# Kernel tuning notes

Measured on AMD Instinct MI355X. Metric: run time of the kernel, lower is better.

The kernel has to match this reference:

```python
import jax, jax.numpy as jnp
import numpy as np

EMBED = 1024
HEADS = 16
HEAD_DIM = EMBED // HEADS


def setup_inputs() -> dict:
    key = jax.random.key(0)
    k_x, k_q, k_k, k_v, k_o, k_b = jax.random.split(key, 6)
    s = 1.0 / np.sqrt(EMBED)
    return {
        "x": jax.random.normal(k_x, (4, 2048, EMBED), dtype=jnp.float32),
        "Wq": jax.random.uniform(k_q, (EMBED, EMBED), jnp.float32, -s, s),
        "Wk": jax.random.uniform(k_k, (EMBED, EMBED), jnp.float32, -s, s),
        "Wv": jax.random.uniform(k_v, (EMBED, EMBED), jnp.float32, -s, s),
        "Wo": jax.random.uniform(k_o, (EMBED, EMBED), jnp.float32, -s, s),
        "bo": jax.random.uniform(k_b, (EMBED,), jnp.float32, -s, s),
    }


def reference(x, Wq, Wk, Wv, Wo, bo):
    B, S, E = x.shape
    H, D = HEADS, HEAD_DIM
    # torch nn.Linear: y = x @ W.T
    q = (x @ Wq.T).reshape(B, S, H, D).transpose(0, 2, 1, 3)  # [B,H,S,D]
    k = (x @ Wk.T).reshape(B, S, H, D).transpose(0, 2, 1, 3)
    v = (x @ Wv.T).reshape(B, S, H, D).transpose(0, 2, 1, 3)
    # NOTE: module scales by sqrt(embed_size), not sqrt(head_dim)
    scores = jnp.einsum("bhqd,bhkd->bhqk", q, k) / jnp.sqrt(jnp.float32(E))
    causal = jnp.triu(jnp.ones((S, S), dtype=bool), k=1)
    scores = jnp.where(causal, -jnp.inf, scores)
    attn = jax.nn.softmax(scores, axis=-1)
    out = jnp.einsum("bhqk,bhkd->bhqd", attn, v)  # [B,H,S,D]
    out = out.transpose(0, 2, 1, 3).reshape(B, S, E)
    return out @ Wo.T + bo
```

## Files before the change

### kernel.cpp

```cpp
#include <hip/hip_runtime.h>


#define E_DIM 1024
#define S_LEN 2048
#define BATCH 4
#define NHEAD 16
#define HDIM  64

using short8 = __attribute__((ext_vector_type(8))) short;
using f32x4  = __attribute__((ext_vector_type(4))) float;

#define GLD16(gp, lp) __builtin_amdgcn_global_load_lds( \
    (const __attribute__((address_space(1))) void*)(gp), \
    (__attribute__((address_space(3))) void*)(lp), 16, 0, 0)

__device__ inline unsigned short f2bf(float f) {
    unsigned int u = __builtin_bit_cast(unsigned int, f);
    u += 0x7FFFu + ((u >> 16) & 1u);
    return (unsigned short)(u >> 16);
}

__global__ __launch_bounds__(256) void cvt_all(
        const float* __restrict__ x,  const float* __restrict__ wq,
        const float* __restrict__ wk, const float* __restrict__ wv,
        const float* __restrict__ wo,
        unsigned short* __restrict__ xb, unsigned short* __restrict__ wb) {
    const int bid = blockIdx.x;
    const float* src;
    unsigned short* dst;
    int blk;
    if (bid < 8192) { src = x; dst = xb; blk = bid; }
    else {
        const int wsel = (bid - 8192) >> 10;
        blk = (bid - 8192) & 1023;
        src = (wsel == 0) ? wq : (wsel == 1) ? wk : (wsel == 2) ? wv : wo;
        dst = wb + (size_t)wsel * 1048576;
    }
    const int i = (blk * 256 + threadIdx.x) * 4;
    float4 v = *reinterpret_cast<const float4*>(src + i);
    ushort4 o;
    o.x = f2bf(v.x); o.y = f2bf(v.y); o.z = f2bf(v.z); o.w = f2bf(v.w);
    *reinterpret_cast<ushort4*>(dst + i) = o;
}

__global__ __launch_bounds__(256) void gemm_qkv(
        const unsigned short* __restrict__ xb,
        const unsigned short* __restrict__ wb,
        unsigned short* __restrict__ qkv) {
    const int z = blockIdx.z;
    const unsigned short* Bw = wb + (size_t)z * (E_DIM * E_DIM);
    unsigned short* Out = qkv + (size_t)z * ((size_t)BATCH * NHEAD * S_LEN * HDIM);
    const int m0 = blockIdx.x * 128, n0 = blockIdx.y * 128;
    const int tid = threadIdx.x;
    const int lane = tid & 63, w = tid >> 6;
    const int wm = w >> 1, wn = w & 1;
    const int col = lane & 15, hi = lane >> 4;

    __shared__ __align__(16) unsigned short Alds[128 * 32];
    __shared__ __align__(16) unsigned short Blds[128 * 32];

    const int srow = tid >> 2;
    const int sc8  = (tid & 3) * 8;
    const int wofs = w * 512;

    f32x4 acc[4][4] = {};

    for (int kt = 0; kt < E_DIM / 32; ++kt) {
        const int k0 = kt * 32;
        GLD16(xb + (size_t)(m0 + srow) * E_DIM + k0 + sc8,       &Alds[wofs]);
        GLD16(xb + (size_t)(m0 + 64 + srow) * E_DIM + k0 + sc8,  &Alds[2048 + wofs]);
        GLD16(Bw + (size_t)(n0 + srow) * E_DIM + k0 + sc8,       &Blds[wofs]);
        GLD16(Bw + (size_t)(n0 + 64 + srow) * E_DIM + k0 + sc8,  &Blds[2048 + wofs]);
        __syncthreads();
        short8 af[4], bf[4];
#pragma unroll
        for (int mt = 0; mt < 4; ++mt)
            af[mt] = *reinterpret_cast<const short8*>(&Alds[(wm * 64 + mt * 16 + col) * 32 + hi * 8]);
#pragma unroll
        for (int nt = 0; nt < 4; ++nt)
            bf[nt] = *reinterpret_cast<const short8*>(&Blds[(wn * 64 + nt * 16 + col) * 32 + hi * 8]);
#pragma unroll
        for (int mt = 0; mt < 4; ++mt)
#pragma unroll
            for (int nt = 0; nt < 4; ++nt)
                acc[mt][nt] = __builtin_amdgcn_mfma_f32_16x16x32_bf16(af[mt], bf[nt], acc[mt][nt], 0, 0, 0);
        __syncthreads();
    }

    const float scale = (z == 0) ? (0.03125f * 1.44269504f) : 1.0f;
#pragma unroll
    for (int mt = 0; mt < 4; ++mt) {
#pragma unroll
        for (int nt = 0; nt < 4; ++nt) {
#pragma unroll
            for (int b = 0; b < 4; ++b) {
                int m = m0 + wm * 64 + mt * 16 + hi * 4 + b;
                int n = n0 + wn * 64 + nt * 16 + col;
                int bidx = m >> 11, s = m & 2047;
                int h = n >> 6, d = n & 63;
                size_t off = (((size_t)(bidx * NHEAD + h)) * S_LEN + s) * HDIM + d;
                Out[off] = f2bf(acc[mt][nt][b] * scale);
            }
        }
    }
}

__global__ __launch_bounds__(512, 4) void attn_fwd(
        const unsigned short* __restrict__ Q,
        const unsigned short* __restrict__ K,
        const unsigned short* __restrict__ V,
        unsigned short* __restrict__ Out) {
    const int g = blockIdx.x;
    const int p = g >> 6;
    const int bh = (g & 7) + ((g >> 3) & 7) * 8;
    const int b_idx = bh >> 4, h = bh & 15;
    const int tid = threadIdx.x, lane = tid & 63, w = tid >> 6;
    const int col = lane & 15, hi = lane >> 4;

    const unsigned short* Qb = Q + (size_t)bh * (S_LEN * HDIM);
    const unsigned short* Kb = K + (size_t)bh * (S_LEN * HDIM);
    const unsigned short* Vb = V + (size_t)bh * (S_LEN * HDIM);

    __shared__ __align__(16) unsigned short Klds[64 * 64];
    __shared__ __align__(16) unsigned short Vt[64 * 64];
    __shared__ __align__(16) unsigned short Plds[8][16 * 64];
    unsigned short* Pl = &Plds[w][0];

    const int kr = tid >> 3, kc8 = (tid & 7) * 8;
    const int ksw = kc8 ^ ((kr & 7) << 3);
    const int vr = tid & 63, vc8 = (tid >> 6) * 8;

#pragma unroll
    for (int pass = 0; pass < 2; ++pass) {
        const int qt = pass ? (15 - p) : p;
        const int nt = 2 * qt + 2;
        const int q0 = qt * 128 + w * 16;

        short8 qf0, qf1;
        {
            const unsigned short* qrow = Qb + (size_t)(q0 + col) * HDIM;
            qf0 = *reinterpret_cast<const short8*>(qrow + hi * 8);
            qf1 = *reinterpret_cast<const short8*>(qrow + 32 + hi * 8);
        }

        f32x4 acc[4] = {};
        float mrun[4], lrun[4];
#pragma unroll
        for (int b = 0; b < 4; ++b) { mrun[b] = -INFINITY; lrun[b] = 0.f; }

        short8 pk = *reinterpret_cast<const short8*>(Kb + (size_t)kr * HDIM + kc8);
        short8 pv = *reinterpret_cast<const short8*>(Vb + (size_t)vr * HDIM + vc8);

        for (int t = 0; t < nt; ++t) {
            const int kv0 = t * 64;
            __syncthreads();
            *reinterpret_cast<short8*>(&Klds[kr * 64 + ksw]) = pk;
#pragma unroll
            for (int j = 0; j < 8; ++j) {
                const int d0 = vc8 + j;
                Vt[d0 * 64 + (vr ^ ((d0 & 7) << 3))] = (unsigned short)pv[j];
            }
            if (t < nt - 1) {
                const int kn = kv0 + 64;
                pk = *reinterpret_cast<const short8*>(Kb + (size_t)(kn + kr) * HDIM + kc8);
                pv = *reinterpret_cast<const short8*>(Vb + (size_t)(kn + vr) * HDIM + vc8);
            }
            __syncthreads();

            if (kv0 <= q0 + 15) {
                f32x4 s[4];
                __builtin_amdgcn_s_setprio(1);
#pragma unroll
                for (int kc = 0; kc < 4; ++kc) {
                    const int row = kc * 16 + col;
                    const int sw = (row & 7) << 3;
                    const unsigned short* kb = Klds + row * 64;
                    short8 kf0 = *reinterpret_cast<const short8*>(kb + ((hi * 8) ^ sw));
                    short8 kf1 = *reinterpret_cast<const short8*>(kb + ((32 + hi * 8) ^ sw));
                    f32x4 z4 = {0.f, 0.f, 0.f, 0.f};
                    z4 = __builtin_amdgcn_mfma_f32_16x16x32_bf16(qf0, kf0, z4, 0, 0, 0);
                    s[kc] = __builtin_amdgcn_mfma_f32_16x16x32_bf16(qf1, kf1, z4, 0, 0, 0);
                }
                __builtin_amdgcn_s_setprio(0);

                if (kv0 + 63 > q0) {
#pragma unroll
                    for (int kc = 0; kc < 4; ++kc) {
                        int kg = kv0 + kc * 16 + col;
#pragma unroll
                        for (int b = 0; b < 4; ++b) {
                            int qg = q0 + hi * 4 + b;
                            if (kg > qg) s[kc][b] = -INFINITY;
                        }
                    }
                }

                float vb[4];
#pragma unroll
                for (int b = 0; b < 4; ++b) {
                    float v = fmaxf(fmaxf(s[0][b], s[1][b]), fmaxf(s[2][b], s[3][b]));
                    v = fmaxf(v, __shfl_xor(v, 1));
                    v = fmaxf(v, __shfl_xor(v, 2));
                    v = fmaxf(v, __shfl_xor(v, 4));
                    v = fmaxf(v, __shfl_xor(v, 8));
                    vb[b] = v;
                }
                bool grow = (vb[0] > mrun[0] + 11.5f) || (vb[1] > mrun[1] + 11.5f) ||
                            (vb[2] > mrun[2] + 11.5f) || (vb[3] > mrun[3] + 11.5f);
                if (__any(grow)) {
#pragma unroll
                    for (int b = 0; b < 4; ++b) {
                        float mnew = fmaxf(mrun[b], vb[b]);
                        float fac = exp2f(mrun[b] - mnew);
                        mrun[b] = mnew;
                        lrun[b] *= fac;
#pragma unroll
                        for (int dt = 0; dt < 4; ++dt) acc[dt][b] *= fac;
                    }
                }
#pragma unroll
                for (int kc = 0; kc < 4; ++kc) {
                    const int c = kc * 16 + col;
#pragma unroll
                    for (int b = 0; b < 4; ++b) {
                        float pp = exp2f(s[kc][b] - mrun[b]);
                        lrun[b] += pp;
                        const int r = hi * 4 + b;
                        Pl[r * 64 + (c ^ ((r & 7) << 3))] = f2bf(pp);
                    }
                }
                const int psw = (col & 7) << 3;
                short8 pf0 = *reinterpret_cast<const short8*>(Pl + col * 64 + ((hi * 8) ^ psw));
                short8 pf1 = *reinterpret_cast<const short8*>(Pl + col * 64 + ((32 + hi * 8) ^ psw));

                __builtin_amdgcn_s_setprio(1);
#pragma unroll
                for (int dt = 0; dt < 4; ++dt) {
                    const int row = dt * 16 + col;
                    const int sw = (row & 7) << 3;
                    const unsigned short* vbp = Vt + row * 64;
                    short8 vf0 = *reinterpret_cast<const short8*>(vbp + ((hi * 8) ^ sw));
                    short8 vf1 = *reinterpret_cast<const short8*>(vbp + ((32 + hi * 8) ^ sw));
                    acc[dt] = __builtin_amdgcn_mfma_f32_16x16x32_bf16(pf0, vf0, acc[dt], 0, 0, 0);
                    acc[dt] = __builtin_amdgcn_mfma_f32_16x16x32_bf16(pf1, vf1, acc[dt], 0, 0, 0);
                }
                __builtin_amdgcn_s_setprio(0);
            }
        }

#pragma unroll
        for (int b = 0; b < 4; ++b) {
            float l = lrun[b];
            l += __shfl_xor(l, 1);
            l += __shfl_xor(l, 2);
            l += __shfl_xor(l, 4);
            l += __shfl_xor(l, 8);
            float inv = 1.0f / l;
            int qg = q0 + hi * 4 + b;
#pragma unroll
            for (int dt = 0; dt < 4; ++dt) {
                size_t off = ((size_t)(b_idx * S_LEN + qg)) * E_DIM + h * HDIM + dt * 16 + col;
                Out[off] = f2bf(acc[dt][b] * inv);
            }
        }
    }
}

__global__ __launch_bounds__(256) void gemm_out(
        const unsigned short* __restrict__ Ab,
        const unsigned short* __restrict__ Bw,
        const float* __restrict__ bias,
        float* __restrict__ Out) {
    const int m0 = blockIdx.x * 128, n0 = blockIdx.y * 128;
    const int tid = threadIdx.x;
    const int lane = tid & 63, w = tid >> 6;
    const int wm = w >> 1, wn = w & 1;
    const int col = lane & 15, hi = lane >> 4;

    __shared__ __align__(16) unsigned short Alds[128 * 32];
    __shared__ __align__(16) unsigned short Blds[128 * 32];

    const int srow = tid >> 2;
    const int sc8  = (tid & 3) * 8;
    const int wofs = w * 512;

    f32x4 acc[4][4] = {};

    for (int kt = 0; kt < E_DIM / 32; ++kt) {
        const int k0 = kt * 32;
        GLD16(Ab + (size_t)(m0 + srow) * E_DIM + k0 + sc8,       &Alds[wofs]);
        GLD16(Ab + (size_t)(m0 + 64 + srow) * E_DIM + k0 + sc8,  &Alds[2048 + wofs]);
        GLD16(Bw + (size_t)(n0 + srow) * E_DIM + k0 + sc8,       &Blds[wofs]);
        GLD16(Bw + (size_t)(n0 + 64 + srow) * E_DIM + k0 + sc8,  &Blds[2048 + wofs]);
        __syncthreads();
        short8 af[4], bf[4];
#pragma unroll
        for (int mt = 0; mt < 4; ++mt)
            af[mt] = *reinterpret_cast<const short8*>(&Alds[(wm * 64 + mt * 16 + col) * 32 + hi * 8]);
#pragma unroll
        for (int nt = 0; nt < 4; ++nt)
            bf[nt] = *reinterpret_cast<const short8*>(&Blds[(wn * 64 + nt * 16 + col) * 32 + hi * 8]);
#pragma unroll
        for (int mt = 0; mt < 4; ++mt)
#pragma unroll
            for (int nt = 0; nt < 4; ++nt)
                acc[mt][nt] = __builtin_amdgcn_mfma_f32_16x16x32_bf16(af[mt], bf[nt], acc[mt][nt], 0, 0, 0);
        __syncthreads();
    }

#pragma unroll
    for (int mt = 0; mt < 4; ++mt) {
#pragma unroll
        for (int nt = 0; nt < 4; ++nt) {
#pragma unroll
            for (int b = 0; b < 4; ++b) {
                int m = m0 + wm * 64 + mt * 16 + hi * 4 + b;
                int n = n0 + wn * 64 + nt * 16 + col;
                Out[(size_t)m * E_DIM + n] = acc[mt][nt][b] + bias[n];
            }
        }
    }
}

extern "C" void kernel_launch(void* const* d_in, const int* in_sizes, int n_in,
                              void* d_out, int out_size, void* d_ws, size_t ws_size,
                              hipStream_t stream) {
    const float* x  = (const float*)d_in[0];
    const float* Wq = (const float*)d_in[1];
    const float* Wk = (const float*)d_in[2];
    const float* Wv = (const float*)d_in[3];
    const float* Wo = (const float*)d_in[4];
    const float* bo = (const float*)d_in[5];
    float* out = (float*)d_out;

    unsigned short* ws   = (unsigned short*)d_ws;
    unsigned short* xb   = ws;
    unsigned short* wb   = xb + (size_t)8192 * 1024;
    unsigned short* qkv  = wb + (size_t)4 * 1024 * 1024;
    unsigned short* attn = qkv + (size_t)3 * 8192 * 1024;

    cvt_all<<<12288, 256, 0, stream>>>(x, Wq, Wk, Wv, Wo, xb, wb);
    gemm_qkv<<<dim3(64, 8, 3), 256, 0, stream>>>(xb, wb, qkv);
    attn_fwd<<<512, 512, 0, stream>>>(qkv, qkv + 8388608, qkv + 2 * 8388608, attn);
    gemm_out<<<dim3(64, 8), 256, 0, stream>>>(attn, wb + 3 * 1048576, bo, out);
}
```

Before: 196.5 us.

## Switch attention to 32x32x16 MFMA with transposed S and register P

Rewrites the attention kernel to compute S^T and O^T with 32x32x16 bf16 MFMAs, so each of 4 waves owns 32 query rows in a 256-thread block. The softmax row statistics become per-lane values, which removes most cross-lane shuffle reductions. P is repacked into MFMA operands through lane-xor-32 shuffles and packed bf16 conversion instead of a round trip through LDS. The P LDS buffer is dropped and the output uses packed 32-bit stores. In exchange, registers per thread go up and there are fewer threads per block to load K and V tiles.

New measurement: 196.9 us. Within noise of the previous version (+0.2%).

```diff
diff --git a/kernel.cpp b/kernel.cpp
--- a/kernel.cpp
+++ b/kernel.cpp
@@ -9,6 +9,8 @@
 
 using short8 = __attribute__((ext_vector_type(8))) short;
 using f32x4  = __attribute__((ext_vector_type(4))) float;
+using f32x16 = __attribute__((ext_vector_type(16))) float;
+using i32x4  = __attribute__((ext_vector_type(4))) int;
 
 #define GLD16(gp, lp) __builtin_amdgcn_global_load_lds( \
     (const __attribute__((address_space(1))) void*)(gp), \
@@ -18,6 +20,12 @@
     unsigned int u = __builtin_bit_cast(unsigned int, f);
     u += 0x7FFFu + ((u >> 16) & 1u);
     return (unsigned short)(u >> 16);
+}
+
+__device__ inline unsigned int cvt_pk_bf16(float a, float b) {
+    unsigned int r;
+    asm("v_cvt_pk_bf16_f32 %0, %1, %2" : "=v"(r) : "v"(a), "v"(b));
+    return r;
 }
 
 __global__ __launch_bounds__(256) void cvt_all(
@@ -105,7 +113,7 @@
     }
 }
 
-__global__ __launch_bounds__(512, 4) void attn_fwd(
+__global__ __launch_bounds__(256, 4) void attn_fwd(
         const unsigned short* __restrict__ Q,
         const unsigned short* __restrict__ K,
         const unsigned short* __restrict__ V,
@@ -115,7 +123,9 @@
     const int bh = (g & 7) + ((g >> 3) & 7) * 8;
     const int b_idx = bh >> 4, h = bh & 15;
     const int tid = threadIdx.x, lane = tid & 63, w = tid >> 6;
-    const int col = lane & 15, hi = lane >> 4;
+    const int l31 = lane & 31, b5 = lane >> 5;
+    const bool lo32 = (b5 == 0);
+    const int rsw = (l31 & 7) << 3;
 
     const unsigned short* Qb = Q + (size_t)bh * (S_LEN * HDIM);
     const unsigned short* Kb = K + (size_t)bh * (S_LEN * HDIM);
@@ -123,8 +133,6 @@
 
     __shared__ __align__(16) unsigned short Klds[64 * 64];
     __shared__ __align__(16) unsigned short Vt[64 * 64];
-    __shared__ __align__(16) unsigned short Plds[8][16 * 64];
-    unsigned short* Pl = &Plds[w][0];
 
     const int kr = tid >> 3, kc8 = (tid & 7) * 8;
     const int ksw = kc8 ^ ((kr & 7) << 3);
@@ -134,134 +142,129 @@
     for (int pass = 0; pass < 2; ++pass) {
         const int qt = pass ? (15 - p) : p;
         const int nt = 2 * qt + 2;
-        const int q0 = qt * 128 + w * 16;
-
-        short8 qf0, qf1;
+        const int q0w = qt * 128 + w * 32;
+        const int qg = q0w + l31;
+
+        short8 qf[4];
         {
-            const unsigned short* qrow = Qb + (size_t)(q0 + col) * HDIM;
-            qf0 = *reinterpret_cast<const short8*>(qrow + hi * 8);
-            qf1 = *reinterpret_cast<const short8*>(qrow + 32 + hi * 8);
-        }
-
-        f32x4 acc[4] = {};
-        float mrun[4], lrun[4];
-#pragma unroll
-        for (int b = 0; b < 4; ++b) { mrun[b] = -INFINITY; lrun[b] = 0.f; }
-
-        short8 pk = *reinterpret_cast<const short8*>(Kb + (size_t)kr * HDIM + kc8);
-        short8 pv = *reinterpret_cast<const short8*>(Vb + (size_t)vr * HDIM + vc8);
+            const unsigned short* qrow = Qb + (size_t)qg * HDIM;
+#pragma unroll
+            for (int dc = 0; dc < 4; ++dc)
+                qf[dc] = *reinterpret_cast<const short8*>(qrow + dc * 16 + b5 * 8);
+        }
+
+        f32x16 ot0 = {}, ot1 = {};
+        float mrun = -INFINITY, lsum = 0.f;
+
+        short8 pk0 = *reinterpret_cast<const short8*>(Kb + (size_t)kr * HDIM + kc8);
+        short8 pk1 = *reinterpret_cast<const short8*>(Kb + (size_t)(32 + kr) * HDIM + kc8);
+        short8 pv0 = *reinterpret_cast<const short8*>(Vb + (size_t)vr * HDIM + vc8);
+        short8 pv1 = *reinterpret_cast<const short8*>(Vb + (size_t)vr * HDIM + vc8 + 32);
 
         for (int t = 0; t < nt; ++t) {
             const int kv0 = t * 64;
             __syncthreads();
-            *reinterpret_cast<short8*>(&Klds[kr * 64 + ksw]) = pk;
+            *reinterpret_cast<short8*>(&Klds[kr * 64 + ksw]) = pk0;
+            *reinterpret_cast<short8*>(&Klds[(kr + 32) * 64 + ksw]) = pk1;
 #pragma unroll
             for (int j = 0; j < 8; ++j) {
                 const int d0 = vc8 + j;
-                Vt[d0 * 64 + (vr ^ ((d0 & 7) << 3))] = (unsigned short)pv[j];
+                const int vsw = vr ^ ((d0 & 7) << 3);
+                Vt[d0 * 64 + vsw]        = (unsigned short)pv0[j];
+                Vt[(d0 + 32) * 64 + vsw] = (unsigned short)pv1[j];
             }
             if (t < nt - 1) {
                 const int kn = kv0 + 64;
-                pk = *reinterpret_cast<const short8*>(Kb + (size_t)(kn + kr) * HDIM + kc8);
-                pv = *reinterpret_cast<const short8*>(Vb + (size_t)(kn + vr) * HDIM + vc8);
+                pk0 = *reinterpret_cast<const short8*>(Kb + (size_t)(kn + kr) * HDIM + kc8);
+                pk1 = *reinterpret_cast<const short8*>(Kb + (size_t)(kn + 32 + kr) * HDIM + kc8);
+                pv0 = *reinterpret_cast<const short8*>(Vb + (size_t)(kn + vr) * HDIM + vc8);
+                pv1 = *reinterpret_cast<const short8*>(Vb + (size_t)(kn + vr) * HDIM + vc8 + 32);
             }
             __syncthreads();
 
-            if (kv0 <= q0 + 15) {
-                f32x4 s[4];
+            if (kv0 <= q0w + 31) {
+                f32x16 st0 = {}, st1 = {};
                 __builtin_amdgcn_s_setprio(1);
 #pragma unroll
-                for (int kc = 0; kc < 4; ++kc) {
-                    const int row = kc * 16 + col;
-                    const int sw = (row & 7) << 3;
-                    const unsigned short* kb = Klds + row * 64;
-                    short8 kf0 = *reinterpret_cast<const short8*>(kb + ((hi * 8) ^ sw));
-                    short8 kf1 = *reinterpret_cast<const short8*>(kb + ((32 + hi * 8) ^ sw));
-                    f32x4 z4 = {0.f, 0.f, 0.f, 0.f};
-                    z4 = __builtin_amdgcn_mfma_f32_16x16x32_bf16(qf0, kf0, z4, 0, 0, 0);
-                    s[kc] = __builtin_amdgcn_mfma_f32_16x16x32_bf16(qf1, kf1, z4, 0, 0, 0);
+                for (int dc = 0; dc < 4; ++dc) {
+                    const int co = dc * 16 + b5 * 8;
+                    short8 kfA = *reinterpret_cast<const short8*>(&Klds[l31 * 64 + (co ^ rsw)]);
+                    short8 kfB = *reinterpret_cast<const short8*>(&Klds[(32 + l31) * 64 + (co ^ rsw)]);
+                    st0 = __builtin_amdgcn_mfma_f32_32x32x16_bf16(kfA, qf[dc], st0, 0, 0, 0);
+                    st1 = __builtin_amdgcn_mfma_f32_32x32x16_bf16(kfB, qf[dc], st1, 0, 0, 0);
                 }
                 __builtin_amdgcn_s_setprio(0);
 
-                if (kv0 + 63 > q0) {
-#pragma unroll
-                    for (int kc = 0; kc < 4; ++kc) {
-                        int kg = kv0 + kc * 16 + col;
-#pragma unroll
-                        for (int b = 0; b < 4; ++b) {
-                            int qg = q0 + hi * 4 + b;
-                            if (kg > qg) s[kc][b] = -INFINITY;
-                        }
+                if (kv0 + 63 > q0w) {
+#pragma unroll
+                    for (int r = 0; r < 16; ++r) {
+                        const int krow = (r & 3) + 8 * (r >> 2) + 4 * b5;
+                        if (kv0 + krow > qg)      st0[r] = -INFINITY;
+                        if (kv0 + 32 + krow > qg) st1[r] = -INFINITY;
                     }
                 }
 
-                float vb[4];
-#pragma unroll
-                for (int b = 0; b < 4; ++b) {
-                    float v = fmaxf(fmaxf(s[0][b], s[1][b]), fmaxf(s[2][b], s[3][b]));
-                    v = fmaxf(v, __shfl_xor(v, 1));
-                    v = fmaxf(v, __shfl_xor(v, 2));
-                    v = fmaxf(v, __shfl_xor(v, 4));
-                    v = fmaxf(v, __shfl_xor(v, 8));
-                    vb[b] = v;
+                float vm = st0[0];
+#pragma unroll
+                for (int r = 1; r < 16; ++r) vm = fmaxf(vm, st0[r]);
+#pragma unroll
+                for (int r = 0; r < 16; ++r) vm = fmaxf(vm, st1[r]);
+                vm = fmaxf(vm, __shfl_xor(vm, 32));
+                if (__any(vm > mrun + 11.5f)) {
+                    const float mnew = fmaxf(mrun, vm);
+                    const float fac = exp2f(mrun - mnew);
+                    mrun = mnew;
+                    lsum *= fac;
+#pragma unroll
+                    for (int r = 0; r < 16; ++r) { ot0[r] *= fac; ot1[r] *= fac; }
                 }
-                bool grow = (vb[0] > mrun[0] + 11.5f) || (vb[1] > mrun[1] + 11.5f) ||
-                            (vb[2] > mrun[2] + 11.5f) || (vb[3] > mrun[3] + 11.5f);
-                if (__any(grow)) {
-#pragma unroll
-                    for (int b = 0; b < 4; ++b) {
-                        float mnew = fmaxf(mrun[b], vb[b]);
-                        float fac = exp2f(mrun[b] - mnew);
-                        mrun[b] = mnew;
-                        lrun[b] *= fac;
-#pragma unroll
-                        for (int dt = 0; dt < 4; ++dt) acc[dt][b] *= fac;
+
+#pragma unroll
+                for (int kc = 0; kc < 4; ++kc) {
+                    const int r0 = (kc & 1) * 8;
+                    float pe[8];
+#pragma unroll
+                    for (int i = 0; i < 8; ++i) {
+                        const float sv = (kc < 2) ? st0[r0 + i] : st1[r0 + i];
+                        pe[i] = exp2f(sv - mrun);
+                        lsum += pe[i];
                     }
+                    const unsigned int W0 = cvt_pk_bf16(pe[0], pe[1]);
+                    const unsigned int W1 = cvt_pk_bf16(pe[2], pe[3]);
+                    const unsigned int W2 = cvt_pk_bf16(pe[4], pe[5]);
+                    const unsigned int W3 = cvt_pk_bf16(pe[6], pe[7]);
+                    const unsigned int t0 = (unsigned int)__shfl_xor((int)W0, 32);
+                    const unsigned int t1 = (unsigned int)__shfl_xor((int)W1, 32);
+                    const unsigned int t2 = (unsigned int)__shfl_xor((int)W2, 32);
+                    const unsigned int t3 = (unsigned int)__shfl_xor((int)W3, 32);
+                    i32x4 wv;
+                    wv[0] = (int)(lo32 ? W0 : t2);
+                    wv[1] = (int)(lo32 ? W1 : t3);
+                    wv[2] = (int)(lo32 ? t0 : W2);
+                    wv[3] = (int)(lo32 ? t1 : W3);
+                    const short8 pf = __builtin_bit_cast(short8, wv);
+
+                    const int co = kc * 16 + b5 * 8;
+                    short8 vf0 = *reinterpret_cast<const short8*>(&Vt[l31 * 64 + (co ^ rsw)]);
+                    short8 vf1 = *reinterpret_cast<const short8*>(&Vt[(32 + l31) * 64 + (co ^ rsw)]);
+                    __builtin_amdgcn_s_setprio(1);
+                    ot0 = __builtin_amdgcn_mfma_f32_32x32x16_bf16(vf0, pf, ot0, 0, 0, 0);
+                    ot1 = __builtin_amdgcn_mfma_f32_32x32x16_bf16(vf1, pf, ot1, 0, 0, 0);
+                    __builtin_amdgcn_s_setprio(0);
                 }
-#pragma unroll
-                for (int kc = 0; kc < 4; ++kc) {
-                    const int c = kc * 16 + col;
-#pragma unroll
-                    for (int b = 0; b < 4; ++b) {
-                        float pp = exp2f(s[kc][b] - mrun[b]);
-                        lrun[b] += pp;
-                        const int r = hi * 4 + b;
-                        Pl[r * 64 + (c ^ ((r & 7) << 3))] = f2bf(pp);
-                    }
-                }
-                const int psw = (col & 7) << 3;
-                short8 pf0 = *reinterpret_cast<const short8*>(Pl + col * 64 + ((hi * 8) ^ psw));
-                short8 pf1 = *reinterpret_cast<const short8*>(Pl + col * 64 + ((32 + hi * 8) ^ psw));
-
-                __builtin_amdgcn_s_setprio(1);
-#pragma unroll
-                for (int dt = 0; dt < 4; ++dt) {
-                    const int row = dt * 16 + col;
-                    const int sw = (row & 7) << 3;
-                    const unsigned short* vbp = Vt + row * 64;
-                    short8 vf0 = *reinterpret_cast<const short8*>(vbp + ((hi * 8) ^ sw));
-                    short8 vf1 = *reinterpret_cast<const short8*>(vbp + ((32 + hi * 8) ^ sw));
-                    acc[dt] = __builtin_amdgcn_mfma_f32_16x16x32_bf16(pf0, vf0, acc[dt], 0, 0, 0);
-                    acc[dt] = __builtin_amdgcn_mfma_f32_16x16x32_bf16(pf1, vf1, acc[dt], 0, 0, 0);
-                }
-                __builtin_amdgcn_s_setprio(0);
-            }
-        }
-
-#pragma unroll
-        for (int b = 0; b < 4; ++b) {
-            float l = lrun[b];
-            l += __shfl_xor(l, 1);
-            l += __shfl_xor(l, 2);
-            l += __shfl_xor(l, 4);
-            l += __shfl_xor(l, 8);
-            float inv = 1.0f / l;
-            int qg = q0 + hi * 4 + b;
-#pragma unroll
-            for (int dt = 0; dt < 4; ++dt) {
-                size_t off = ((size_t)(b_idx * S_LEN + qg)) * E_DIM + h * HDIM + dt * 16 + col;
-                Out[off] = f2bf(acc[dt][b] * inv);
-            }
+            }
+        }
+
+        const float lfull = lsum + __shfl_xor(lsum, 32);
+        const float inv = 1.0f / lfull;
+        const size_t base = ((size_t)(b_idx * S_LEN + qg)) * E_DIM + h * HDIM;
+#pragma unroll
+        for (int r2 = 0; r2 < 8; ++r2) {
+            const int d0 = 2 * (r2 & 1) + 8 * (r2 >> 1) + 4 * b5;
+            const unsigned int u0 = cvt_pk_bf16(ot0[2 * r2] * inv, ot0[2 * r2 + 1] * inv);
+            const unsigned int u1 = cvt_pk_bf16(ot1[2 * r2] * inv, ot1[2 * r2 + 1] * inv);
+            *reinterpret_cast<unsigned int*>(const_cast<unsigned short*>(Out) + base + d0) = u0;
+            *reinterpret_cast<unsigned int*>(const_cast<unsigned short*>(Out) + base + 32 + d0) = u1;
         }
     }
 }
@@ -341,6 +344,6 @@
 
     cvt_all<<<12288, 256, 0, stream>>>(x, Wq, Wk, Wv, Wo, xb, wb);
     gemm_qkv<<<dim3(64, 8, 3), 256, 0, stream>>>(xb, wb, qkv);
-    attn_fwd<<<512, 512, 0, stream>>>(qkv, qkv + 8388608, qkv + 2 * 8388608, attn);
+    attn_fwd<<<512, 256, 0, stream>>>(qkv, qkv + 8388608, qkv + 2 * 8388608, attn);
     gemm_out<<<dim3(64, 8), 256, 0, stream>>>(attn, wb + 3 * 1048576, bo, out);
 }
```
